# Optimization experiments

Measured on AMD Instinct MI355X. Metric: run time of the kernel, lower is better.

The kernel has to match this reference:

```python
import jax, jax.numpy as jnp
import numpy as np

ALPHA = 0.2  # leaky-relu negative slope
N_NODES = 50000
IN_F = 256
OUT_F = 64
N_EDGES = 1600000


def setup_inputs() -> dict:
    key = jax.random.key(0)
    k1, k2, k3, k4 = jax.random.split(key, 4)
    x = jax.random.normal(k1, (N_NODES, IN_F), dtype=jnp.float32)
    # xavier_normal-ish scales for params
    W = jax.random.normal(k2, (IN_F, OUT_F), dtype=jnp.float32) * (1.414 * (2.0 / (IN_F + OUT_F)) ** 0.5)
    a = jax.random.normal(k3, (1, 2 * OUT_F), dtype=jnp.float32) * (1.414 * (2.0 / (1 + 2 * OUT_F)) ** 0.5)
    edge_index = jax.random.randint(k4, (2, N_EDGES), 0, N_NODES, dtype=jnp.int64)
    return {"x": x, "W": W, "a": a, "edge_index": edge_index}


def reference(x, W, a, edge_index):
    N = x.shape[0]
    src = edge_index[0]  # row index of sparse adjacency (aggregation target)
    dst = edge_index[1]  # column index (neighbor being gathered)
    h = x @ W  # [N, out]
    out_f = h.shape[1]
    # a @ cat(h[src], h[dst]) == (h @ a1)[src] + (h @ a2)[dst]
    a1 = a[0, :out_f]
    a2 = a[0, out_f:]
    s_src = h @ a1  # [N]
    s_dst = h @ a2  # [N]
    score = s_src[src] + s_dst[dst]  # [E]
    edge_e = jnp.exp(-jax.nn.leaky_relu(score, negative_slope=ALPHA))  # [E]
    # e_rowsum[i] = sum_{e: src==i} edge_e[e]
    e_rowsum = jax.ops.segment_sum(edge_e, src, num_segments=N)  # [N]
    # h_prime[i] = sum_{e: src==i} edge_e[e] * h[dst[e]]
    h_prime = jax.ops.segment_sum(edge_e[:, None] * h[dst], src, num_segments=N)  # [N, out]
    h_prime = h_prime / e_rowsum[:, None]
    return jax.nn.elu(h_prime)
```

## Files before the change

kernel.cpp:

```cpp
#include <hip/hip_runtime.h>
#include <hip/hip_bf16.h>
#include <hip/hip_fp16.h>


#define ALPHA 0.2f
#define KDIM 256
#define FDIM 64
#define BIN_CHUNK 4096
#define BUCKET_CAP 4096

typedef __bf16 bf16x8 __attribute__((ext_vector_type(8)));
typedef float f32x4 __attribute__((ext_vector_type(4)));
typedef unsigned int u32;
typedef unsigned short u16;

__global__ __launch_bounds__(256) void gat_wt_kernel(
    const float* __restrict__ W, __hip_bfloat16* __restrict__ w_t,
    int* __restrict__ bcur)
{
    const int t = blockIdx.x * 256 + threadIdx.x;
    if (t < KDIM * FDIM) {
        const int k = t >> 6;
        const int n = t & 63;
        w_t[n * KDIM + k] = __float2bfloat16(W[t]);
    }
    if (t < 1024) bcur[t] = 0;
}

__global__ __launch_bounds__(256) void gat_gemm_bin_kernel(
    const float* __restrict__ x, const __hip_bfloat16* __restrict__ w_tp,
    const float* __restrict__ a, __hip_bfloat16* __restrict__ h_bf,
    float* __restrict__ s_src, float* __restrict__ s_dst,
    const int* __restrict__ srcA, const int* __restrict__ dstA,
    int* __restrict__ bcur, u32* __restrict__ pair,
    int N, int E, int NBU, int NBLK)
{
    __shared__ int hist[1024];
    __shared__ int lcur[1024];

    const int t = threadIdx.x;

    if ((int)blockIdx.x < NBLK) {
        for (int j = t; j < 1024; j += 256) hist[j] = 0;
        __syncthreads();
        const int base = blockIdx.x * BIN_CHUNK;
        const int cnt = min(BIN_CHUNK, E - base);
        for (int i = t; i < cnt; i += 256)
            atomicAdd(&hist[srcA[base + i] >> 6], 1);
        __syncthreads();
        for (int j = t; j < NBU; j += 256) {
            const int v = hist[j];
            lcur[j] = v ? (j * BUCKET_CAP + atomicAdd(&bcur[j], v)) : 0;
        }
        __syncthreads();
        for (int i = t; i < cnt; i += 256) {
            const int s = srcA[base + i];
            const int d = dstA[base + i];
            const int pos = atomicAdd(&lcur[s >> 6], 1);
            pair[pos] = ((u32)(s & 63) << 16) | (u32)d;
        }
        return;
    }

    const int gb = (int)blockIdx.x - NBLK;
    const int lane = t & 63;
    const int wv = t >> 6;
    const int m0 = gb * 128 + wv * 32;
    const int c = lane & 15;
    const int q = lane >> 4;

    const int r0 = m0 + c;
    const int r1 = m0 + 16 + c;
    const float* xp0 = x + (long)(r0 < N ? r0 : N - 1) * KDIM;
    const float* xp1 = x + (long)(r1 < N ? r1 : N - 1) * KDIM;
    const __bf16* wt = (const __bf16*)w_tp;

    f32x4 acc[2][4];
#pragma unroll
    for (int rt = 0; rt < 2; ++rt)
#pragma unroll
        for (int ct = 0; ct < 4; ++ct) acc[rt][ct] = (f32x4){0.f, 0.f, 0.f, 0.f};

#pragma unroll 2
    for (int kc = 0; kc < 8; ++kc) {
        const int k0 = kc * 32 + q * 8;
        const float4 xa0 = *(const float4*)(xp0 + k0);
        const float4 xb0 = *(const float4*)(xp0 + k0 + 4);
        const float4 xa1 = *(const float4*)(xp1 + k0);
        const float4 xb1 = *(const float4*)(xp1 + k0 + 4);
        bf16x8 af0, af1;
        af0[0] = (__bf16)xa0.x; af0[1] = (__bf16)xa0.y;
        af0[2] = (__bf16)xa0.z; af0[3] = (__bf16)xa0.w;
        af0[4] = (__bf16)xb0.x; af0[5] = (__bf16)xb0.y;
        af0[6] = (__bf16)xb0.z; af0[7] = (__bf16)xb0.w;
        af1[0] = (__bf16)xa1.x; af1[1] = (__bf16)xa1.y;
        af1[2] = (__bf16)xa1.z; af1[3] = (__bf16)xa1.w;
        af1[4] = (__bf16)xb1.x; af1[5] = (__bf16)xb1.y;
        af1[6] = (__bf16)xb1.z; af1[7] = (__bf16)xb1.w;
#pragma unroll
        for (int ct = 0; ct < 4; ++ct) {
            const bf16x8 bf = *(const bf16x8*)(wt + (ct * 16 + c) * KDIM + k0);
            acc[0][ct] = __builtin_amdgcn_mfma_f32_16x16x32_bf16(af0, bf, acc[0][ct], 0, 0, 0);
            acc[1][ct] = __builtin_amdgcn_mfma_f32_16x16x32_bf16(af1, bf, acc[1][ct], 0, 0, 0);
        }
    }

    float a1c[4], a2c[4];
#pragma unroll
    for (int ct = 0; ct < 4; ++ct) {
        a1c[ct] = a[ct * 16 + c];
        a2c[ct] = a[FDIM + ct * 16 + c];
    }

#pragma unroll
    for (int rt = 0; rt < 2; ++rt) {
        const int mb = m0 + rt * 16;
        float s1r[4], s2r[4];
#pragma unroll
        for (int reg = 0; reg < 4; ++reg) {
            float s1 = 0.f, s2 = 0.f;
#pragma unroll
            for (int ct = 0; ct < 4; ++ct) {
                s1 += acc[rt][ct][reg] * a1c[ct];
                s2 += acc[rt][ct][reg] * a2c[ct];
            }
            s1r[reg] = s1; s2r[reg] = s2;
        }
#pragma unroll
        for (int off = 1; off < 16; off <<= 1) {
#pragma unroll
            for (int reg = 0; reg < 4; ++reg) {
                s1r[reg] += __shfl_xor(s1r[reg], off);
                s2r[reg] += __shfl_xor(s2r[reg], off);
            }
        }
#pragma unroll
        for (int reg = 0; reg < 4; ++reg) {
            const int row = mb + q * 4 + reg;
            if (row < N) {
#pragma unroll
                for (int ct = 0; ct < 4; ++ct)
                    h_bf[(long)row * FDIM + ct * 16 + c] = __float2bfloat16(acc[rt][ct][reg]);
                if (c == 0) { s_src[row] = s1r[reg]; s_dst[row] = s2r[reg]; }
            }
        }
    }
}

__global__ __launch_bounds__(512) void gat_sortgather_kernel(
    const u32* __restrict__ pair, const int* __restrict__ bcur,
    const float* __restrict__ s_src, const float* __restrict__ s_dst,
    const __hip_bfloat16* __restrict__ h_bf, float* __restrict__ out, int N)
{
    __shared__ u32 chunk[BUCKET_CAP];
    __shared__ u32 slds[BUCKET_CAP];
    __shared__ int cur[64];
    __shared__ int nst[64];
    __shared__ int nen[64];
    __shared__ float ssl[64];

    const int b = blockIdx.x;
    const int t = threadIdx.x;
    const int s0 = b << 6;
    const int abase = b * BUCKET_CAP;
    const int n = min(bcur[b], BUCKET_CAP);

    if (t < 64) {
        cur[t] = 0;
        ssl[t] = (s0 + t < N) ? s_src[s0 + t] : 0.f;
    }
    __syncthreads();
    for (int i = t; i < n; i += 512) {
        const u32 p = pair[abase + i];
        chunk[i] = p;
        atomicAdd(&cur[p >> 16], 1);
    }
    __syncthreads();
    if (t < 64) {
        const int v = cur[t];
        int incl = v;
#pragma unroll
        for (int off = 1; off < 64; off <<= 1) {
            const int nv = __shfl_up(incl, off);
            if (t >= off) incl += nv;
        }
        const int excl = incl - v;
        nst[t] = excl;
        nen[t] = excl + v;
        cur[t] = excl;
    }
    __syncthreads();
    for (int i = t; i < n; i += 512) {
        const u32 p = chunk[i];
        const int sl = p >> 16;
        const int d = (int)(p & 0xFFFFu);
        const int slot = atomicAdd(&cur[sl], 1);
        const float sc = ssl[sl] + s_dst[d];
        const float lr = sc > 0.f ? sc : ALPHA * sc;
        const float wgt = __expf(-lr);
        const u32 wh = (u32)__half_as_ushort(__float2half(wgt));
        slds[slot] = (u32)d | (wh << 16);
    }
    __syncthreads();

    const int wv = t >> 6;
    const int lane = t & 63;
    const int q = lane >> 3;
    const int c = lane & 7;
    const __bf16* hb = (const __bf16*)h_bf;

    for (int nl = wv; nl < 64; nl += 8) {
        const int node = s0 + nl;
        if (node >= N) break;
        const int start = nst[nl];
        const int end = nen[nl];

        float acc0[8], acc1[8];
#pragma unroll
        for (int j = 0; j < 8; ++j) { acc0[j] = 0.f; acc1[j] = 0.f; }
        float wsum0 = 0.f, wsum1 = 0.f;

        int e = start + q;
        for (; e + 8 < end; e += 16) {
            const u32 p0 = slds[e];
            const u32 p1 = slds[e + 8];
            const int d0 = (int)(p0 & 0xFFFFu);
            const int d1 = (int)(p1 & 0xFFFFu);
            const bf16x8 hv0 = *(const bf16x8*)(hb + (long)d0 * FDIM + 8 * c);
            const bf16x8 hv1 = *(const bf16x8*)(hb + (long)d1 * FDIM + 8 * c);
            const float w0 = __half2float(__ushort_as_half((u16)(p0 >> 16)));
            const float w1 = __half2float(__ushort_as_half((u16)(p1 >> 16)));
#pragma unroll
            for (int j = 0; j < 8; ++j) {
                acc0[j] += w0 * (float)hv0[j];
                acc1[j] += w1 * (float)hv1[j];
            }
            wsum0 += w0;
            wsum1 += w1;
        }
        if (e < end) {
            const u32 p0 = slds[e];
            const int d0 = (int)(p0 & 0xFFFFu);
            const bf16x8 hv0 = *(const bf16x8*)(hb + (long)d0 * FDIM + 8 * c);
            const float w0 = __half2float(__ushort_as_half((u16)(p0 >> 16)));
#pragma unroll
            for (int j = 0; j < 8; ++j) acc0[j] += w0 * (float)hv0[j];
            wsum0 += w0;
        }

        float acc[8];
#pragma unroll
        for (int j = 0; j < 8; ++j) acc[j] = acc0[j] + acc1[j];
        float wsum = wsum0 + wsum1;

#pragma unroll
        for (int off = 8; off < 64; off <<= 1) {
#pragma unroll
            for (int j = 0; j < 8; ++j) acc[j] += __shfl_xor(acc[j], off);
            wsum += __shfl_xor(wsum, off);
        }

        if (q == 0) {
            const float inv = 1.0f / wsum;
            float o[8];
#pragma unroll
            for (int j = 0; j < 8; ++j) {
                const float v = acc[j] * inv;
                o[j] = v > 0.f ? v : expm1f(v);
            }
            float* op = &out[(long)node * FDIM + 8 * c];
            *(float4*)op = make_float4(o[0], o[1], o[2], o[3]);
            *(float4*)(op + 4) = make_float4(o[4], o[5], o[6], o[7]);
        }
    }
}

extern "C" void kernel_launch(void* const* d_in, const int* in_sizes, int n_in,
                              void* d_out, int out_size, void* d_ws, size_t ws_size,
                              hipStream_t stream) {
    const float* x = (const float*)d_in[0];
    const float* W = (const float*)d_in[1];
    const float* a = (const float*)d_in[2];
    const int* ei  = (const int*)d_in[3];

    const int N = in_sizes[0] / KDIM;
    const int E = in_sizes[3] / 2;
    const int NBU = (N + 63) >> 6;
    const int NBLK = (E + BIN_CHUNK - 1) / BIN_CHUNK;
    const int GB = (N + 127) / 128;
    const int* srcA = ei;
    const int* dstA = ei + E;

    __hip_bfloat16* h_bf = (__hip_bfloat16*)d_ws;
    __hip_bfloat16* w_t  = h_bf + (size_t)N * FDIM;
    float* s_src = (float*)(w_t + KDIM * FDIM);
    float* s_dst = s_src + N;
    int* bcur    = (int*)(s_dst + N);
    u32* pair    = (u32*)(bcur + 1024);
    float* out   = (float*)d_out;

    gat_wt_kernel<<<dim3((KDIM * FDIM + 255) / 256), dim3(256), 0, stream>>>(
        W, w_t, bcur);

    gat_gemm_bin_kernel<<<dim3(NBLK + GB), dim3(256), 0, stream>>>(
        x, w_t, a, h_bf, s_src, s_dst, srcA, dstA, bcur, pair, N, E, NBU, NBLK);

    gat_sortgather_kernel<<<dim3(NBU), dim3(512), 0, stream>>>(
        pair, bcur, s_src, s_dst, h_bf, out, N);
}
```

Measured before the change: 170.0 us.

## Widen GEMM/bin blocks to 512 threads and unroll gather loop four-way

The fused GEMM+binning kernel now runs 512 threads per block. Each GEMM wave handles 16 rows instead of 32, and the binning loops stride by 512. The gather loop in the sort-gather kernel adds a four-way unrolled path with four independent accumulators, so more h-row loads are in flight per wave. This trades extra registers, which may reduce occupancy, for more memory-level parallelism and less per-wave work.

```diff
diff --git a/kernel.cpp b/kernel.cpp
--- a/kernel.cpp
+++ b/kernel.cpp
@@ -27,7 +27,7 @@
     if (t < 1024) bcur[t] = 0;
 }
 
-__global__ __launch_bounds__(256) void gat_gemm_bin_kernel(
+__global__ __launch_bounds__(512) void gat_gemm_bin_kernel(
     const float* __restrict__ x, const __hip_bfloat16* __restrict__ w_tp,
     const float* __restrict__ a, __hip_bfloat16* __restrict__ h_bf,
     float* __restrict__ s_src, float* __restrict__ s_dst,
@@ -41,19 +41,19 @@
     const int t = threadIdx.x;
 
     if ((int)blockIdx.x < NBLK) {
-        for (int j = t; j < 1024; j += 256) hist[j] = 0;
+        for (int j = t; j < 1024; j += 512) hist[j] = 0;
         __syncthreads();
         const int base = blockIdx.x * BIN_CHUNK;
         const int cnt = min(BIN_CHUNK, E - base);
-        for (int i = t; i < cnt; i += 256)
+        for (int i = t; i < cnt; i += 512)
             atomicAdd(&hist[srcA[base + i] >> 6], 1);
         __syncthreads();
-        for (int j = t; j < NBU; j += 256) {
+        for (int j = t; j < NBU; j += 512) {
             const int v = hist[j];
             lcur[j] = v ? (j * BUCKET_CAP + atomicAdd(&bcur[j], v)) : 0;
         }
         __syncthreads();
-        for (int i = t; i < cnt; i += 256) {
+        for (int i = t; i < cnt; i += 512) {
             const int s = srcA[base + i];
             const int d = dstA[base + i];
             const int pos = atomicAdd(&lcur[s >> 6], 1);
@@ -65,43 +65,32 @@
     const int gb = (int)blockIdx.x - NBLK;
     const int lane = t & 63;
     const int wv = t >> 6;
-    const int m0 = gb * 128 + wv * 32;
+    const int m0 = gb * 128 + wv * 16;
     const int c = lane & 15;
     const int q = lane >> 4;
 
     const int r0 = m0 + c;
-    const int r1 = m0 + 16 + c;
     const float* xp0 = x + (long)(r0 < N ? r0 : N - 1) * KDIM;
-    const float* xp1 = x + (long)(r1 < N ? r1 : N - 1) * KDIM;
     const __bf16* wt = (const __bf16*)w_tp;
 
-    f32x4 acc[2][4];
-#pragma unroll
-    for (int rt = 0; rt < 2; ++rt)
-#pragma unroll
-        for (int ct = 0; ct < 4; ++ct) acc[rt][ct] = (f32x4){0.f, 0.f, 0.f, 0.f};
+    f32x4 acc[4];
+#pragma unroll
+    for (int ct = 0; ct < 4; ++ct) acc[ct] = (f32x4){0.f, 0.f, 0.f, 0.f};
 
 #pragma unroll 2
     for (int kc = 0; kc < 8; ++kc) {
         const int k0 = kc * 32 + q * 8;
         const float4 xa0 = *(const float4*)(xp0 + k0);
         const float4 xb0 = *(const float4*)(xp0 + k0 + 4);
-        const float4 xa1 = *(const float4*)(xp1 + k0);
-        const float4 xb1 = *(const float4*)(xp1 + k0 + 4);
-        bf16x8 af0, af1;
+        bf16x8 af0;
         af0[0] = (__bf16)xa0.x; af0[1] = (__bf16)xa0.y;
         af0[2] = (__bf16)xa0.z; af0[3] = (__bf16)xa0.w;
         af0[4] = (__bf16)xb0.x; af0[5] = (__bf16)xb0.y;
         af0[6] = (__bf16)xb0.z; af0[7] = (__bf16)xb0.w;
-        af1[0] = (__bf16)xa1.x; af1[1] = (__bf16)xa1.y;
-        af1[2] = (__bf16)xa1.z; af1[3] = (__bf16)xa1.w;
-        af1[4] = (__bf16)xb1.x; af1[5] = (__bf16)xb1.y;
-        af1[6] = (__bf16)xb1.z; af1[7] = (__bf16)xb1.w;
 #pragma unroll
         for (int ct = 0; ct < 4; ++ct) {
             const bf16x8 bf = *(const bf16x8*)(wt + (ct * 16 + c) * KDIM + k0);
-            acc[0][ct] = __builtin_amdgcn_mfma_f32_16x16x32_bf16(af0, bf, acc[0][ct], 0, 0, 0);
-            acc[1][ct] = __builtin_amdgcn_mfma_f32_16x16x32_bf16(af1, bf, acc[1][ct], 0, 0, 0);
+            acc[ct] = __builtin_amdgcn_mfma_f32_16x16x32_bf16(af0, bf, acc[ct], 0, 0, 0);
         }
     }
 
@@ -112,37 +101,33 @@
         a2c[ct] = a[FDIM + ct * 16 + c];
     }
 
-#pragma unroll
-    for (int rt = 0; rt < 2; ++rt) {
-        const int mb = m0 + rt * 16;
-        float s1r[4], s2r[4];
+    float s1r[4], s2r[4];
+#pragma unroll
+    for (int reg = 0; reg < 4; ++reg) {
+        float s1 = 0.f, s2 = 0.f;
+#pragma unroll
+        for (int ct = 0; ct < 4; ++ct) {
+            s1 += acc[ct][reg] * a1c[ct];
+            s2 += acc[ct][reg] * a2c[ct];
+        }
+        s1r[reg] = s1; s2r[reg] = s2;
+    }
+#pragma unroll
+    for (int off = 1; off < 16; off <<= 1) {
 #pragma unroll
         for (int reg = 0; reg < 4; ++reg) {
-            float s1 = 0.f, s2 = 0.f;
-#pragma unroll
-            for (int ct = 0; ct < 4; ++ct) {
-                s1 += acc[rt][ct][reg] * a1c[ct];
-                s2 += acc[rt][ct][reg] * a2c[ct];
-            }
-            s1r[reg] = s1; s2r[reg] = s2;
-        }
-#pragma unroll
-        for (int off = 1; off < 16; off <<= 1) {
-#pragma unroll
-            for (int reg = 0; reg < 4; ++reg) {
-                s1r[reg] += __shfl_xor(s1r[reg], off);
-                s2r[reg] += __shfl_xor(s2r[reg], off);
-            }
-        }
-#pragma unroll
-        for (int reg = 0; reg < 4; ++reg) {
-            const int row = mb + q * 4 + reg;
-            if (row < N) {
-#pragma unroll
-                for (int ct = 0; ct < 4; ++ct)
-                    h_bf[(long)row * FDIM + ct * 16 + c] = __float2bfloat16(acc[rt][ct][reg]);
-                if (c == 0) { s_src[row] = s1r[reg]; s_dst[row] = s2r[reg]; }
-            }
+            s1r[reg] += __shfl_xor(s1r[reg], off);
+            s2r[reg] += __shfl_xor(s2r[reg], off);
+        }
+    }
+#pragma unroll
+    for (int reg = 0; reg < 4; ++reg) {
+        const int row = m0 + q * 4 + reg;
+        if (row < N) {
+#pragma unroll
+            for (int ct = 0; ct < 4; ++ct)
+                h_bf[(long)row * FDIM + ct * 16 + c] = __float2bfloat16(acc[ct][reg]);
+            if (c == 0) { s_src[row] = s1r[reg]; s_dst[row] = s2r[reg]; }
         }
     }
 }
@@ -215,12 +200,40 @@
         const int start = nst[nl];
         const int end = nen[nl];
 
-        float acc0[8], acc1[8];
-#pragma unroll
-        for (int j = 0; j < 8; ++j) { acc0[j] = 0.f; acc1[j] = 0.f; }
-        float wsum0 = 0.f, wsum1 = 0.f;
+        float acc0[8], acc1[8], acc2[8], acc3[8];
+#pragma unroll
+        for (int j = 0; j < 8; ++j) {
+            acc0[j] = 0.f; acc1[j] = 0.f; acc2[j] = 0.f; acc3[j] = 0.f;
+        }
+        float wsum0 = 0.f, wsum1 = 0.f, wsum2 = 0.f, wsum3 = 0.f;
 
         int e = start + q;
+        for (; e + 24 < end; e += 32) {
+            const u32 p0 = slds[e];
+            const u32 p1 = slds[e + 8];
+            const u32 p2 = slds[e + 16];
+            const u32 p3 = slds[e + 24];
+            const int d0 = (int)(p0 & 0xFFFFu);
+            const int d1 = (int)(p1 & 0xFFFFu);
+            const int d2 = (int)(p2 & 0xFFFFu);
+            const int d3 = (int)(p3 & 0xFFFFu);
+            const bf16x8 hv0 = *(const bf16x8*)(hb + (long)d0 * FDIM + 8 * c);
+            const bf16x8 hv1 = *(const bf16x8*)(hb + (long)d1 * FDIM + 8 * c);
+            const bf16x8 hv2 = *(const bf16x8*)(hb + (long)d2 * FDIM + 8 * c);
+            const bf16x8 hv3 = *(const bf16x8*)(hb + (long)d3 * FDIM + 8 * c);
+            const float w0 = __half2float(__ushort_as_half((u16)(p0 >> 16)));
+            const float w1 = __half2float(__ushort_as_half((u16)(p1 >> 16)));
+            const float w2 = __half2float(__ushort_as_half((u16)(p2 >> 16)));
+            const float w3 = __half2float(__ushort_as_half((u16)(p3 >> 16)));
+#pragma unroll
+            for (int j = 0; j < 8; ++j) {
+                acc0[j] += w0 * (float)hv0[j];
+                acc1[j] += w1 * (float)hv1[j];
+                acc2[j] += w2 * (float)hv2[j];
+                acc3[j] += w3 * (float)hv3[j];
+            }
+            wsum0 += w0; wsum1 += w1; wsum2 += w2; wsum3 += w3;
+        }
         for (; e + 8 < end; e += 16) {
             const u32 p0 = slds[e];
             const u32 p1 = slds[e + 8];
@@ -235,8 +248,7 @@
                 acc0[j] += w0 * (float)hv0[j];
                 acc1[j] += w1 * (float)hv1[j];
             }
-            wsum0 += w0;
-            wsum1 += w1;
+            wsum0 += w0; wsum1 += w1;
         }
         if (e < end) {
             const u32 p0 = slds[e];
@@ -250,8 +262,8 @@
 
         float acc[8];
 #pragma unroll
-        for (int j = 0; j < 8; ++j) acc[j] = acc0[j] + acc1[j];
-        float wsum = wsum0 + wsum1;
+        for (int j = 0; j < 8; ++j) acc[j] = (acc0[j] + acc1[j]) + (acc2[j] + acc3[j]);
+        float wsum = (wsum0 + wsum1) + (wsum2 + wsum3);
 
 #pragma unroll
         for (int off = 8; off < 64; off <<= 1) {
@@ -302,7 +314,7 @@
     gat_wt_kernel<<<dim3((KDIM * FDIM + 255) / 256), dim3(256), 0, stream>>>(
         W, w_t, bcur);
 
-    gat_gemm_bin_kernel<<<dim3(NBLK + GB), dim3(256), 0, stream>>>(
+    gat_gemm_bin_kernel<<<dim3(NBLK + GB), dim3(512), 0, stream>>>(
         x, w_t, a, h_bf, s_src, s_dst, srcA, dstA, bcur, pair, N, E, NBU, NBLK);
 
     gat_sortgather_kernel<<<dim3(NBU), dim3(512), 0, stream>>>(
```

New measurement: 195.9 us. +15.2%, slower.

## Halve GEMM row tile and split each sort-gather bucket across two blocks

Applied to the files above, without the earlier changes.

The GEMM part now has each wave compute 16 rows instead of 32, which doubles the GEMM block count. The sort-gather kernel now launches two 256-thread blocks per 64-node bucket. Each block filters the bucket's pairs for its 32 nodes and reads pair from global memory twice instead of staging it in LDS. The aim is more parallelism and lower LDS use per block, so occupancy rises. In exchange, each bucket's pairs are read redundantly, and any half-bucket with more than HCAP edges is silently truncated.

```diff
diff --git a/kernel.cpp b/kernel.cpp
--- a/kernel.cpp
+++ b/kernel.cpp
@@ -8,6 +8,7 @@
 #define FDIM 64
 #define BIN_CHUNK 4096
 #define BUCKET_CAP 4096
+#define HCAP 2304
 
 typedef __bf16 bf16x8 __attribute__((ext_vector_type(8)));
 typedef float f32x4 __attribute__((ext_vector_type(4)));
@@ -65,43 +66,32 @@
     const int gb = (int)blockIdx.x - NBLK;
     const int lane = t & 63;
     const int wv = t >> 6;
-    const int m0 = gb * 128 + wv * 32;
+    const int m0 = gb * 64 + wv * 16;
     const int c = lane & 15;
     const int q = lane >> 4;
 
     const int r0 = m0 + c;
-    const int r1 = m0 + 16 + c;
     const float* xp0 = x + (long)(r0 < N ? r0 : N - 1) * KDIM;
-    const float* xp1 = x + (long)(r1 < N ? r1 : N - 1) * KDIM;
     const __bf16* wt = (const __bf16*)w_tp;
 
-    f32x4 acc[2][4];
-#pragma unroll
-    for (int rt = 0; rt < 2; ++rt)
-#pragma unroll
-        for (int ct = 0; ct < 4; ++ct) acc[rt][ct] = (f32x4){0.f, 0.f, 0.f, 0.f};
+    f32x4 acc[4];
+#pragma unroll
+    for (int ct = 0; ct < 4; ++ct) acc[ct] = (f32x4){0.f, 0.f, 0.f, 0.f};
 
 #pragma unroll 2
     for (int kc = 0; kc < 8; ++kc) {
         const int k0 = kc * 32 + q * 8;
         const float4 xa0 = *(const float4*)(xp0 + k0);
         const float4 xb0 = *(const float4*)(xp0 + k0 + 4);
-        const float4 xa1 = *(const float4*)(xp1 + k0);
-        const float4 xb1 = *(const float4*)(xp1 + k0 + 4);
-        bf16x8 af0, af1;
+        bf16x8 af0;
         af0[0] = (__bf16)xa0.x; af0[1] = (__bf16)xa0.y;
         af0[2] = (__bf16)xa0.z; af0[3] = (__bf16)xa0.w;
         af0[4] = (__bf16)xb0.x; af0[5] = (__bf16)xb0.y;
         af0[6] = (__bf16)xb0.z; af0[7] = (__bf16)xb0.w;
-        af1[0] = (__bf16)xa1.x; af1[1] = (__bf16)xa1.y;
-        af1[2] = (__bf16)xa1.z; af1[3] = (__bf16)xa1.w;
-        af1[4] = (__bf16)xb1.x; af1[5] = (__bf16)xb1.y;
-        af1[6] = (__bf16)xb1.z; af1[7] = (__bf16)xb1.w;
 #pragma unroll
         for (int ct = 0; ct < 4; ++ct) {
             const bf16x8 bf = *(const bf16x8*)(wt + (ct * 16 + c) * KDIM + k0);
-            acc[0][ct] = __builtin_amdgcn_mfma_f32_16x16x32_bf16(af0, bf, acc[0][ct], 0, 0, 0);
-            acc[1][ct] = __builtin_amdgcn_mfma_f32_16x16x32_bf16(af1, bf, acc[1][ct], 0, 0, 0);
+            acc[ct] = __builtin_amdgcn_mfma_f32_16x16x32_bf16(af0, bf, acc[ct], 0, 0, 0);
         }
     }
 
@@ -112,94 +102,93 @@
         a2c[ct] = a[FDIM + ct * 16 + c];
     }
 
-#pragma unroll
-    for (int rt = 0; rt < 2; ++rt) {
-        const int mb = m0 + rt * 16;
-        float s1r[4], s2r[4];
+    float s1r[4], s2r[4];
+#pragma unroll
+    for (int reg = 0; reg < 4; ++reg) {
+        float s1 = 0.f, s2 = 0.f;
+#pragma unroll
+        for (int ct = 0; ct < 4; ++ct) {
+            s1 += acc[ct][reg] * a1c[ct];
+            s2 += acc[ct][reg] * a2c[ct];
+        }
+        s1r[reg] = s1; s2r[reg] = s2;
+    }
+#pragma unroll
+    for (int off = 1; off < 16; off <<= 1) {
 #pragma unroll
         for (int reg = 0; reg < 4; ++reg) {
-            float s1 = 0.f, s2 = 0.f;
-#pragma unroll
-            for (int ct = 0; ct < 4; ++ct) {
-                s1 += acc[rt][ct][reg] * a1c[ct];
-                s2 += acc[rt][ct][reg] * a2c[ct];
-            }
-            s1r[reg] = s1; s2r[reg] = s2;
-        }
-#pragma unroll
-        for (int off = 1; off < 16; off <<= 1) {
-#pragma unroll
-            for (int reg = 0; reg < 4; ++reg) {
-                s1r[reg] += __shfl_xor(s1r[reg], off);
-                s2r[reg] += __shfl_xor(s2r[reg], off);
-            }
-        }
-#pragma unroll
-        for (int reg = 0; reg < 4; ++reg) {
-            const int row = mb + q * 4 + reg;
-            if (row < N) {
-#pragma unroll
-                for (int ct = 0; ct < 4; ++ct)
-                    h_bf[(long)row * FDIM + ct * 16 + c] = __float2bfloat16(acc[rt][ct][reg]);
-                if (c == 0) { s_src[row] = s1r[reg]; s_dst[row] = s2r[reg]; }
-            }
-        }
-    }
-}
-
-__global__ __launch_bounds__(512) void gat_sortgather_kernel(
+            s1r[reg] += __shfl_xor(s1r[reg], off);
+            s2r[reg] += __shfl_xor(s2r[reg], off);
+        }
+    }
+#pragma unroll
+    for (int reg = 0; reg < 4; ++reg) {
+        const int row = m0 + q * 4 + reg;
+        if (row < N) {
+#pragma unroll
+            for (int ct = 0; ct < 4; ++ct)
+                h_bf[(long)row * FDIM + ct * 16 + c] = __float2bfloat16(acc[ct][reg]);
+            if (c == 0) { s_src[row] = s1r[reg]; s_dst[row] = s2r[reg]; }
+        }
+    }
+}
+
+__global__ __launch_bounds__(256) void gat_sortgather_kernel(
     const u32* __restrict__ pair, const int* __restrict__ bcur,
     const float* __restrict__ s_src, const float* __restrict__ s_dst,
     const __hip_bfloat16* __restrict__ h_bf, float* __restrict__ out, int N)
 {
-    __shared__ u32 chunk[BUCKET_CAP];
-    __shared__ u32 slds[BUCKET_CAP];
-    __shared__ int cur[64];
-    __shared__ int nst[64];
-    __shared__ int nen[64];
-    __shared__ float ssl[64];
-
-    const int b = blockIdx.x;
+    __shared__ u32 slds[HCAP];
+    __shared__ int cur[32];
+    __shared__ int nst[32];
+    __shared__ int nen[32];
+    __shared__ float ssl[32];
+
+    const int b = (int)blockIdx.x >> 1;
+    const int hf = (int)blockIdx.x & 1;
     const int t = threadIdx.x;
-    const int s0 = b << 6;
+    const int s0 = (b << 6) + (hf << 5);
     const int abase = b * BUCKET_CAP;
     const int n = min(bcur[b], BUCKET_CAP);
-
-    if (t < 64) {
+    const int slo = hf << 5;
+
+    if (t < 32) {
         cur[t] = 0;
         ssl[t] = (s0 + t < N) ? s_src[s0 + t] : 0.f;
     }
     __syncthreads();
-    for (int i = t; i < n; i += 512) {
-        const u32 p = pair[abase + i];
-        chunk[i] = p;
-        atomicAdd(&cur[p >> 16], 1);
-    }
-    __syncthreads();
-    if (t < 64) {
+    for (int i = t; i < n; i += 256) {
+        const int sl = (int)(pair[abase + i] >> 16);
+        if ((sl >> 5) == hf) atomicAdd(&cur[sl & 31], 1);
+    }
+    __syncthreads();
+    if (t < 32) {
         const int v = cur[t];
         int incl = v;
 #pragma unroll
-        for (int off = 1; off < 64; off <<= 1) {
+        for (int off = 1; off < 32; off <<= 1) {
             const int nv = __shfl_up(incl, off);
             if (t >= off) incl += nv;
         }
         const int excl = incl - v;
         nst[t] = excl;
-        nen[t] = excl + v;
+        nen[t] = min(excl + v, HCAP);
         cur[t] = excl;
     }
     __syncthreads();
-    for (int i = t; i < n; i += 512) {
-        const u32 p = chunk[i];
-        const int sl = p >> 16;
+    for (int i = t; i < n; i += 256) {
+        const u32 p = pair[abase + i];
+        const int sl = (int)(p >> 16);
+        if ((sl >> 5) != hf) continue;
         const int d = (int)(p & 0xFFFFu);
-        const int slot = atomicAdd(&cur[sl], 1);
-        const float sc = ssl[sl] + s_dst[d];
-        const float lr = sc > 0.f ? sc : ALPHA * sc;
-        const float wgt = __expf(-lr);
-        const u32 wh = (u32)__half_as_ushort(__float2half(wgt));
-        slds[slot] = (u32)d | (wh << 16);
+        const int slot = atomicAdd(&cur[sl & 31], 1);
+        if (slot < HCAP) {
+            const float sc = ssl[sl & 31] + s_dst[d];
+            const float lr = sc > 0.f ? sc : ALPHA * sc;
+            const float wgt = __expf(-lr);
+            const u32 wh = (u32)__half_as_ushort(__float2half(wgt));
+            slds[slot] = (u32)d | (wh << 16);
+        }
     }
     __syncthreads();
 
@@ -209,7 +198,7 @@
     const int c = lane & 7;
     const __bf16* hb = (const __bf16*)h_bf;
 
-    for (int nl = wv; nl < 64; nl += 8) {
+    for (int nl = wv; nl < 32; nl += 4) {
         const int node = s0 + nl;
         if (node >= N) break;
         const int start = nst[nl];
@@ -287,7 +276,7 @@
     const int E = in_sizes[3] / 2;
     const int NBU = (N + 63) >> 6;
     const int NBLK = (E + BIN_CHUNK - 1) / BIN_CHUNK;
-    const int GB = (N + 127) / 128;
+    const int GB = (N + 63) / 64;
     const int* srcA = ei;
     const int* dstA = ei + E;
 
@@ -305,6 +294,6 @@
     gat_gemm_bin_kernel<<<dim3(NBLK + GB), dim3(256), 0, stream>>>(
         x, w_t, a, h_bf, s_src, s_dst, srcA, dstA, bcur, pair, N, E, NBU, NBLK);
 
-    gat_sortgather_kernel<<<dim3(NBU), dim3(512), 0, stream>>>(
+    gat_sortgather_kernel<<<dim3(NBU * 2), dim3(256), 0, stream>>>(
         pair, bcur, s_src, s_dst, h_bf, out, N);
 }
```

Result: slower. 180.4 us (+6.2%).
